# Optimization experiments

Hardware: AMD Instinct MI355X
Metric: run time of the kernel (lower is better)

Reference implementation:

```python
import jax, jax.numpy as jnp
import numpy as np

KS = 3
OFF = (KS - 1) // 2
KS2 = KS * KS


def _windows(xp, H, W):
    """xp: [..., H+KS-1, W+KS-1] -> [..., H, W, KS, KS] with flat index i = x*KS + y."""
    cols = [xp[..., x:x + H, y:y + W] for x in range(KS) for y in range(KS)]
    w = jnp.stack(cols, axis=-1)                      # [..., H, W, KS*KS]
    return w.reshape(w.shape[:-1] + (KS, KS))


def setup_inputs() -> dict:
    key = jax.random.key(0)
    k1, k2, k3, k4 = jax.random.split(key, 4)
    B, C, H = 8, 3, 512
    img = jax.random.uniform(k1, (B, C, H, H), dtype=jnp.float32) * 255.0
    noise = jax.random.uniform(k2, (B, C, H + 2 * OFF, H + 2 * OFF), dtype=jnp.float32)
    ids_sel = jax.random.randint(k3, (B,), 0, 2) > 0          # ~p selection mask
    ids_dilation_sel = jax.random.randint(k4, (B,), 0, 2) > 0  # ~p_mix mix mask
    return {"img": img, "noise": noise, "ids_sel": ids_sel,
            "ids_dilation_sel": ids_dilation_sel}


def reference(img, noise, ids_sel, ids_dilation_sel):
    B, C, H, W = img.shape
    imgf = img.astype(jnp.float32)
    # pad + additive uniform noise
    img_p = jnp.pad(imgf, ((0, 0), (0, 0), (OFF, OFF), (OFF, OFF))) + noise
    img_e = _windows(img_p, H, W)                     # [B,C,H,W,KS,KS]
    mean = img_e.mean(axis=(4, 5), keepdims=True)
    std = jnp.std(img_e, axis=(4, 5), ddof=1, keepdims=True)  # unbiased
    w = jnp.exp(-(img_e - mean) ** 2 / (2.0 * std ** 2))
    w3 = w.min(axis=1, keepdims=True)                 # [B,1,H,W,KS,KS]
    # first weighted average (sums channels in numerator, like the torch code)
    num = (img_e * w3).sum(axis=(1, 4, 5))            # [B,H,W]
    den = w3.sum(axis=(4, 5))[:, 0]                   # [B,H,W]
    img_r = num / den
    # sort-based pixel mixing: pick argmin (erosion) or argmax (dilation) index
    img_r_p = jnp.pad(img_r, ((0, 0), (OFF, OFF), (OFF, OFF)))
    img_r_e = _windows(img_r_p, H, W).reshape(B, H, W, KS2)
    ids_min = jnp.argmin(img_r_e, axis=3)
    ids_max = jnp.argmax(img_r_e, axis=3)
    ids_mix = jnp.where(ids_dilation_sel[:, None, None], ids_max, ids_min)
    w_flat = w3.reshape(B, H, W, KS2)
    w_mod = jnp.take_along_axis(w_flat, ids_mix[..., None], axis=3)[..., 0]  # [B,H,W]
    # second windowed weighted-average pass with the mixed weights
    w_mod_p = jnp.pad(w_mod, ((0, 0), (OFF, OFF), (OFF, OFF)))
    w_mod_e = _windows(w_mod_p, H, W)[:, None]        # [B,1,H,W,KS,KS]
    img_mod = (img_e * w_mod_e).sum(axis=(4, 5)) / w_mod_e.sum(axis=(4, 5))  # [B,C,H,W]
    out = jnp.where(ids_sel[:, None, None, None], img_mod, imgf)
    return out.astype(jnp.uint8)
```

## Files before the change

kernel.cpp:

```cpp
#include <hip/hip_runtime.h>
#include <hip/hip_fp16.h>

#define HH 512
#define WD 512
#define HP 514
#define BN 8
#define CN 3

#define TH 16
#define TW 32

#define SP_ROWS (TH + 6)
#define SP_COLS (TW + 6)
#define SR_ROWS (TH + 4)
#define SR_COLS (TW + 4)
#define SR_PITCH (SR_COLS + 1)
#define WM_ROWS (TH + 2)
#define WM_COLS (TW + 2)
#define WM_PITCH (WM_COLS + 1)
#define W9_STRIDE 10

__device__ __forceinline__ int load_flag(const int* __restrict__ p, int b) {
    bool all01 = true;
#pragma unroll
    for (int i = 0; i < BN; ++i) {
        int v = p[i];
        all01 = all01 && (v == 0 || v == 1);
    }
    if (all01) return p[b];
    const unsigned char* pb = (const unsigned char*)p;
    return pb[b] != 0;
}

__device__ __forceinline__ float fast_rcp(float x) {
    return __builtin_amdgcn_rcpf(x);
}

template <int P>
__device__ __forceinline__ void p2_pixel(const float4 (&col)[3][3], int r, int cc,
                                         bool hok, int w,
                                         float* __restrict__ sr,
                                         __half* __restrict__ w9) {
    float val = 0.f;
    if (hok && (unsigned)w < (unsigned)WD) {
        float sx = 0.f, sy = 0.f, sz = 0.f;
#pragma unroll
        for (int k = 0; k < 9; ++k) {
            const float4 tp = col[(k % 3 + P) % 3][k / 3];
            sx += tp.x; sy += tp.y; sz += tp.z;
        }
        float mx = sx * (1.f / 9.f), my = sy * (1.f / 9.f), mz = sz * (1.f / 9.f);
        float sdx = 0.f, sdy = 0.f, sdz = 0.f;
#pragma unroll
        for (int k = 0; k < 9; ++k) {
            const float4 tp = col[(k % 3 + P) % 3][k / 3];
            float dx = tp.x - mx, dy = tp.y - my, dz = tp.z - mz;
            sdx += dx * dx; sdy += dy * dy; sdz += dz * dz;
        }
        float ivx = 4.f * fast_rcp(sdx);
        float ivy = 4.f * fast_rcp(sdy);
        float ivz = 4.f * fast_rcp(sdz);
        float wk[9];
        float num = 0.f, den = 0.f;
#pragma unroll
        for (int k = 0; k < 9; ++k) {
            const float4 tp = col[(k % 3 + P) % 3][k / 3];
            float dx = tp.x - mx, dy = tp.y - my, dz = tp.z - mz;
            float txx = dx * dx * ivx, tyy = dy * dy * ivy, tzz = dz * dz * ivz;
            float m = fmaxf(txx, fmaxf(tyy, tzz));
            wk[k] = __expf(-m);
            num += (tp.x + tp.y + tp.z) * wk[k];
            den += wk[k];
        }
        val = num * fast_rcp(den);
        if (r >= 1 && r < SR_ROWS - 1 && cc >= 1 && cc < SR_COLS - 1) {
            int pix = (r - 1) * WM_COLS + (cc - 1);
            unsigned int* wp = (unsigned int*)&w9[pix * W9_STRIDE];
#pragma unroll
            for (int k = 0; k < 4; ++k) {
                __half2 h2 = __floats2half2_rn(wk[2 * k], wk[2 * k + 1]);
                wp[k] = *(unsigned int*)&h2;
            }
            w9[pix * W9_STRIDE + 8] = __float2half_rn(wk[8]);
        }
    }
    sr[r * SR_PITCH + cc] = val;
}

__global__ __launch_bounds__(256) void fused(const float* __restrict__ img,
                                             const float* __restrict__ noise,
                                             const int* __restrict__ ids_sel,
                                             const int* __restrict__ ids_dil,
                                             int* __restrict__ out) {
    int lin = blockIdx.x + 16 * blockIdx.y + 512 * blockIdx.z;
    int xcd = lin & 7;
    int m = lin >> 3;
    int b = m >> 6;
    int within = m & 63;
    int band = (xcd + b) & 7;
    int tl = band * 64 + within;
    int by = tl >> 4, bx = tl & 15;
    int h0 = by * TH, w0 = bx * TW;
    int t = threadIdx.x;

    if (!load_flag(ids_sel, b)) {
        int r = t >> 4, lx = (t & 15) << 1;
#pragma unroll
        for (int c = 0; c < CN; ++c) {
            const float* im = img + (size_t)(b * CN + c) * HH * WD;
            int* op = out + (size_t)(b * CN + c) * HH * WD;
            float2 v = *(const float2*)&im[(h0 + r) * WD + w0 + lx];
            int2 ov;
            ov.x = ((int)v.x) & 255;
            ov.y = ((int)v.y) & 255;
            __builtin_nontemporal_store(*(const long long*)&ov,
                                        (long long*)&op[(h0 + r) * WD + w0 + lx]);
        }
        return;
    }
    bool dil = load_flag(ids_dil, b) != 0;

    __shared__ float4 sp4[SP_ROWS * SP_COLS];
    __shared__ float sr[SR_ROWS * SR_PITCH];
    __shared__ float swm[WM_ROWS * WM_PITCH];
    __shared__ __align__(4) __half w9[WM_ROWS * WM_COLS * W9_STRIDE];

    {
        const float* nz = noise + (size_t)b * CN * HP * HP;
        const float* im = img + (size_t)b * CN * HH * WD;
        for (int idx = t; idx < SP_ROWS * SP_COLS; idx += 256) {
            int r = idx / SP_COLS, cc = idx - r * SP_COLS;
            int ip = h0 - 2 + r, jp = w0 - 2 + cc;
            ip = ip < 0 ? 0 : (ip > HP - 1 ? HP - 1 : ip);
            jp = jp < 0 ? 0 : (jp > HP - 1 ? HP - 1 : jp);
            bool in = (ip >= 1 && ip <= HH && jp >= 1 && jp <= WD);
            int no = ip * HP + jp;
            int io = (ip - 1) * WD + (jp - 1);
            float4 v;
            v.x = nz[no] + (in ? im[io] : 0.f);
            v.y = nz[HP * HP + no] + (in ? im[HH * WD + io] : 0.f);
            v.z = nz[2 * HP * HP + no] + (in ? im[2 * HH * WD + io] : 0.f);
            v.w = 0.f;
            sp4[idx] = v;
        }
    }
    __syncthreads();

    if (t < 240) {
        int r = t / 12;
        int s = t - r * 12;
        int cc0 = 3 * s;
        int h = h0 - 2 + r;
        bool hok = (h >= 0 && h < HH);
        float4 col[3][3];
#pragma unroll
        for (int j = 0; j < 3; ++j)
#pragma unroll
            for (int i = 0; i < 3; ++i)
                col[j][i] = sp4[(r + i) * SP_COLS + cc0 + j];
        p2_pixel<0>(col, r, cc0 + 0, hok, w0 - 2 + cc0 + 0, sr, w9);
#pragma unroll
        for (int i = 0; i < 3; ++i) col[0][i] = sp4[(r + i) * SP_COLS + cc0 + 3];
        p2_pixel<1>(col, r, cc0 + 1, hok, w0 - 2 + cc0 + 1, sr, w9);
#pragma unroll
        for (int i = 0; i < 3; ++i) col[1][i] = sp4[(r + i) * SP_COLS + cc0 + 4];
        p2_pixel<2>(col, r, cc0 + 2, hok, w0 - 2 + cc0 + 2, sr, w9);
    }
    __syncthreads();

    for (int idx = t; idx < WM_ROWS * WM_COLS; idx += 256) {
        int r = idx / WM_COLS, cc = idx - r * WM_COLS;
        int h = h0 - 1 + r, w = w0 - 1 + cc;
        float wmv = 0.f;
        if (h >= 0 && h < HH && w >= 0 && w < WD) {
            float rv[9];
#pragma unroll
            for (int k = 0; k < 9; ++k)
                rv[k] = sr[(r + k / 3) * SR_PITCH + cc + k % 3];
            int amin = 0, amax = 0;
            float vmin = rv[0], vmax = rv[0];
#pragma unroll
            for (int k = 1; k < 9; ++k) {
                if (rv[k] < vmin) { vmin = rv[k]; amin = k; }
                if (rv[k] > vmax) { vmax = rv[k]; amax = k; }
            }
            int ksel = dil ? amax : amin;
            wmv = __half2float(w9[idx * W9_STRIDE + ksel]);
        }
        swm[r * WM_PITCH + cc] = wmv;
    }
    __syncthreads();

    {
        int ly = t >> 4;
        int lx = (t & 15) << 1;
        float4 c4[3][3];
#pragma unroll
        for (int j = 0; j < 3; ++j)
#pragma unroll
            for (int i = 0; i < 3; ++i)
                c4[j][i] = sp4[(ly + 2 + i) * SP_COLS + lx + 2 + j];
        float ws[4][3];
#pragma unroll
        for (int j = 0; j < 4; ++j)
#pragma unroll
            for (int i = 0; i < 3; ++i)
                ws[j][i] = swm[(ly + i) * WM_PITCH + lx + j];
        int2 o0, o1, o2;
        {
            float den = 0.f, nx = 0.f, ny = 0.f, nz2 = 0.f;
#pragma unroll
            for (int k = 0; k < 9; ++k) {
                const float wkk = ws[k % 3][k / 3];
                const float4 tp = c4[k % 3][k / 3];
                den += wkk;
                nx += tp.x * wkk; ny += tp.y * wkk; nz2 += tp.z * wkk;
            }
            float rden = 1.f / den;
            o0.x = ((int)(nx * rden)) & 255;
            o1.x = ((int)(ny * rden)) & 255;
            o2.x = ((int)(nz2 * rden)) & 255;
        }
#pragma unroll
        for (int i = 0; i < 3; ++i) c4[0][i] = sp4[(ly + 2 + i) * SP_COLS + lx + 5];
        {
            float den = 0.f, nx = 0.f, ny = 0.f, nz2 = 0.f;
#pragma unroll
            for (int k = 0; k < 9; ++k) {
                const float wkk = ws[k % 3 + 1][k / 3];
                const float4 tp = c4[(k % 3 + 1) % 3][k / 3];
                den += wkk;
                nx += tp.x * wkk; ny += tp.y * wkk; nz2 += tp.z * wkk;
            }
            float rden = 1.f / den;
            o0.y = ((int)(nx * rden)) & 255;
            o1.y = ((int)(ny * rden)) & 255;
            o2.y = ((int)(nz2 * rden)) & 255;
        }
        size_t o = ((size_t)b * CN * HH + h0 + ly) * WD + w0 + lx;
        __builtin_nontemporal_store(*(const long long*)&o0, (long long*)&out[o]);
        __builtin_nontemporal_store(*(const long long*)&o1,
                                    (long long*)&out[o + (size_t)HH * WD]);
        __builtin_nontemporal_store(*(const long long*)&o2,
                                    (long long*)&out[o + 2 * (size_t)HH * WD]);
    }
}

extern "C" void kernel_launch(void* const* d_in, const int* in_sizes, int n_in,
                              void* d_out, int out_size, void* d_ws, size_t ws_size,
                              hipStream_t stream) {
    const float* img   = (const float*)d_in[0];
    const float* noise = (const float*)d_in[1];
    const int* ids_sel = (const int*)d_in[2];
    const int* ids_dil = (const int*)d_in[3];
    int* out = (int*)d_out;

    dim3 grid(WD / TW, HH / TH, BN);
    fused<<<grid, 256, 0, stream>>>(img, noise, ids_sel, ids_dil, out);
}
```

Before: 110.8 us.

## Shrink LDS footprint, batch nontemporal loads, and raise occupancy target

Drops the separate shared buffer for first-pass results and stores them in the unused w lane of the padded float4 tile. It also stores the mixed weights in half precision, which cuts LDS per block. The tile staging loop is restructured to issue all global loads (now nontemporal) for four iterations before any LDS stores, and launch bounds request 6 blocks per CU. The goal is higher occupancy and more memory-level parallelism. The risks are register pressure from the batched loads and the new occupancy hint, and extra LDS bank conflicts from the strided w-lane access.

New measurement: 111.3 us. No clear change (+0.5%).

```diff
diff --git a/kernel.cpp b/kernel.cpp
--- a/kernel.cpp
+++ b/kernel.cpp
@@ -14,12 +14,13 @@
 #define SP_COLS (TW + 6)
 #define SR_ROWS (TH + 4)
 #define SR_COLS (TW + 4)
-#define SR_PITCH (SR_COLS + 1)
 #define WM_ROWS (TH + 2)
 #define WM_COLS (TW + 2)
 #define WM_PITCH (WM_COLS + 1)
 #define W9_STRIDE 10
 
+typedef float f2v __attribute__((ext_vector_type(2)));
+
 __device__ __forceinline__ int load_flag(const int* __restrict__ p, int b) {
     bool all01 = true;
 #pragma unroll
@@ -36,10 +37,14 @@
     return __builtin_amdgcn_rcpf(x);
 }
 
+__device__ __forceinline__ float nt_load(const float* p) {
+    return __builtin_nontemporal_load(p);
+}
+
 template <int P>
 __device__ __forceinline__ void p2_pixel(const float4 (&col)[3][3], int r, int cc,
                                          bool hok, int w,
-                                         float* __restrict__ sr,
+                                         float* __restrict__ spw,
                                          __half* __restrict__ w9) {
     float val = 0.f;
     if (hok && (unsigned)w < (unsigned)WD) {
@@ -84,14 +89,14 @@
             w9[pix * W9_STRIDE + 8] = __float2half_rn(wk[8]);
         }
     }
-    sr[r * SR_PITCH + cc] = val;
-}
-
-__global__ __launch_bounds__(256) void fused(const float* __restrict__ img,
-                                             const float* __restrict__ noise,
-                                             const int* __restrict__ ids_sel,
-                                             const int* __restrict__ ids_dil,
-                                             int* __restrict__ out) {
+    spw[(r * SP_COLS + cc) * 4 + 3] = val;
+}
+
+__global__ __launch_bounds__(256, 6) void fused(const float* __restrict__ img,
+                                                const float* __restrict__ noise,
+                                                const int* __restrict__ ids_sel,
+                                                const int* __restrict__ ids_dil,
+                                                int* __restrict__ out) {
     int lin = blockIdx.x + 16 * blockIdx.y + 512 * blockIdx.z;
     int xcd = lin & 7;
     int m = lin >> 3;
@@ -109,7 +114,7 @@
         for (int c = 0; c < CN; ++c) {
             const float* im = img + (size_t)(b * CN + c) * HH * WD;
             int* op = out + (size_t)(b * CN + c) * HH * WD;
-            float2 v = *(const float2*)&im[(h0 + r) * WD + w0 + lx];
+            f2v v = __builtin_nontemporal_load((const f2v*)&im[(h0 + r) * WD + w0 + lx]);
             int2 ov;
             ov.x = ((int)v.x) & 255;
             ov.y = ((int)v.y) & 255;
@@ -121,27 +126,47 @@
     bool dil = load_flag(ids_dil, b) != 0;
 
     __shared__ float4 sp4[SP_ROWS * SP_COLS];
-    __shared__ float sr[SR_ROWS * SR_PITCH];
-    __shared__ float swm[WM_ROWS * WM_PITCH];
+    __shared__ __half swm[WM_ROWS * WM_PITCH];
     __shared__ __align__(4) __half w9[WM_ROWS * WM_COLS * W9_STRIDE];
+    float* spw = (float*)sp4;
 
     {
         const float* nz = noise + (size_t)b * CN * HP * HP;
         const float* im = img + (size_t)b * CN * HH * WD;
-        for (int idx = t; idx < SP_ROWS * SP_COLS; idx += 256) {
-            int r = idx / SP_COLS, cc = idx - r * SP_COLS;
-            int ip = h0 - 2 + r, jp = w0 - 2 + cc;
-            ip = ip < 0 ? 0 : (ip > HP - 1 ? HP - 1 : ip);
-            jp = jp < 0 ? 0 : (jp > HP - 1 ? HP - 1 : jp);
-            bool in = (ip >= 1 && ip <= HH && jp >= 1 && jp <= WD);
-            int no = ip * HP + jp;
-            int io = (ip - 1) * WD + (jp - 1);
-            float4 v;
-            v.x = nz[no] + (in ? im[io] : 0.f);
-            v.y = nz[HP * HP + no] + (in ? im[HH * WD + io] : 0.f);
-            v.z = nz[2 * HP * HP + no] + (in ? im[2 * HH * WD + io] : 0.f);
-            v.w = 0.f;
-            sp4[idx] = v;
+        float a0[4], a1[4], a2[4], b0[4], b1[4], b2[4];
+        int sidx[4];
+        bool act[4];
+#pragma unroll
+        for (int q = 0; q < 4; ++q) {
+            int idx = t + q * 256;
+            act[q] = idx < SP_ROWS * SP_COLS;
+            sidx[q] = idx;
+            if (act[q]) {
+                int r = idx / SP_COLS, cc = idx - r * SP_COLS;
+                int ip = h0 - 2 + r, jp = w0 - 2 + cc;
+                ip = ip < 0 ? 0 : (ip > HP - 1 ? HP - 1 : ip);
+                jp = jp < 0 ? 0 : (jp > HP - 1 ? HP - 1 : jp);
+                bool in = (ip >= 1 && ip <= HH && jp >= 1 && jp <= WD);
+                int no = ip * HP + jp;
+                int io = (ip - 1) * WD + (jp - 1);
+                a0[q] = nt_load(nz + no);
+                a1[q] = nt_load(nz + HP * HP + no);
+                a2[q] = nt_load(nz + 2 * HP * HP + no);
+                b0[q] = in ? nt_load(im + io) : 0.f;
+                b1[q] = in ? nt_load(im + HH * WD + io) : 0.f;
+                b2[q] = in ? nt_load(im + 2 * HH * WD + io) : 0.f;
+            }
+        }
+#pragma unroll
+        for (int q = 0; q < 4; ++q) {
+            if (act[q]) {
+                float4 v;
+                v.x = a0[q] + b0[q];
+                v.y = a1[q] + b1[q];
+                v.z = a2[q] + b2[q];
+                v.w = 0.f;
+                sp4[sidx[q]] = v;
+            }
         }
     }
     __syncthreads();
@@ -158,25 +183,25 @@
 #pragma unroll
             for (int i = 0; i < 3; ++i)
                 col[j][i] = sp4[(r + i) * SP_COLS + cc0 + j];
-        p2_pixel<0>(col, r, cc0 + 0, hok, w0 - 2 + cc0 + 0, sr, w9);
+        p2_pixel<0>(col, r, cc0 + 0, hok, w0 - 2 + cc0 + 0, spw, w9);
 #pragma unroll
         for (int i = 0; i < 3; ++i) col[0][i] = sp4[(r + i) * SP_COLS + cc0 + 3];
-        p2_pixel<1>(col, r, cc0 + 1, hok, w0 - 2 + cc0 + 1, sr, w9);
+        p2_pixel<1>(col, r, cc0 + 1, hok, w0 - 2 + cc0 + 1, spw, w9);
 #pragma unroll
         for (int i = 0; i < 3; ++i) col[1][i] = sp4[(r + i) * SP_COLS + cc0 + 4];
-        p2_pixel<2>(col, r, cc0 + 2, hok, w0 - 2 + cc0 + 2, sr, w9);
+        p2_pixel<2>(col, r, cc0 + 2, hok, w0 - 2 + cc0 + 2, spw, w9);
     }
     __syncthreads();
 
     for (int idx = t; idx < WM_ROWS * WM_COLS; idx += 256) {
         int r = idx / WM_COLS, cc = idx - r * WM_COLS;
         int h = h0 - 1 + r, w = w0 - 1 + cc;
-        float wmv = 0.f;
+        __half wmv = __ushort_as_half((unsigned short)0);
         if (h >= 0 && h < HH && w >= 0 && w < WD) {
             float rv[9];
 #pragma unroll
             for (int k = 0; k < 9; ++k)
-                rv[k] = sr[(r + k / 3) * SR_PITCH + cc + k % 3];
+                rv[k] = spw[((r + k / 3) * SP_COLS + cc + k % 3) * 4 + 3];
             int amin = 0, amax = 0;
             float vmin = rv[0], vmax = rv[0];
 #pragma unroll
@@ -185,7 +210,7 @@
                 if (rv[k] > vmax) { vmax = rv[k]; amax = k; }
             }
             int ksel = dil ? amax : amin;
-            wmv = __half2float(w9[idx * W9_STRIDE + ksel]);
+            wmv = w9[idx * W9_STRIDE + ksel];
         }
         swm[r * WM_PITCH + cc] = wmv;
     }
@@ -205,7 +230,7 @@
         for (int j = 0; j < 4; ++j)
 #pragma unroll
             for (int i = 0; i < 3; ++i)
-                ws[j][i] = swm[(ly + i) * WM_PITCH + lx + j];
+                ws[j][i] = __half2float(swm[(ly + i) * WM_PITCH + lx + j]);
         int2 o0, o1, o2;
         {
             float den = 0.f, nx = 0.f, ny = 0.f, nz2 = 0.f;
```

## Process two vertical tiles per block, prefetching second tile's loads into registers

Applied to the files above, without the earlier changes.

Each block now handles two vertically adjacent 16x32 tiles, halving the grid. The global loads for the second tile are issued into registers before phases 3 and 4 of the first tile run, so their latency overlaps with compute. The results are written to shared memory once the first tile is finished. Launch bounds now request 4 blocks per SM. This raises register pressure (24 prefetch floats per thread) and gives fewer blocks for load balancing, and the halo rows between the two tiles are still reloaded rather than reused.

Measured after the change: 110.6 us. About the same (-0.2%).

```diff
diff --git a/kernel.cpp b/kernel.cpp
--- a/kernel.cpp
+++ b/kernel.cpp
@@ -12,6 +12,7 @@
 
 #define SP_ROWS (TH + 6)
 #define SP_COLS (TW + 6)
+#define SP_N (SP_ROWS * SP_COLS)
 #define SR_ROWS (TH + 4)
 #define SR_COLS (TW + 4)
 #define SR_PITCH (SR_COLS + 1)
@@ -20,6 +21,8 @@
 #define WM_PITCH (WM_COLS + 1)
 #define W9_STRIDE 10
 
+typedef float f2v __attribute__((ext_vector_type(2)));
+
 __device__ __forceinline__ int load_flag(const int* __restrict__ p, int b) {
     bool all01 = true;
 #pragma unroll
@@ -34,6 +37,51 @@
 
 __device__ __forceinline__ float fast_rcp(float x) {
     return __builtin_amdgcn_rcpf(x);
+}
+
+struct P1R {
+    float a0[4], a1[4], a2[4];
+    float b0[4], b1[4], b2[4];
+};
+
+__device__ __forceinline__ void p1_issue(const float* __restrict__ nz,
+                                         const float* __restrict__ im,
+                                         int h0, int w0, int t, P1R& R) {
+#pragma unroll
+    for (int q = 0; q < 4; ++q) {
+        int idx = t + q * 256;
+        if (idx < SP_N) {
+            int r = idx / SP_COLS, cc = idx - r * SP_COLS;
+            int ip = h0 - 2 + r, jp = w0 - 2 + cc;
+            ip = ip < 0 ? 0 : (ip > HP - 1 ? HP - 1 : ip);
+            jp = jp < 0 ? 0 : (jp > HP - 1 ? HP - 1 : jp);
+            bool in = (ip >= 1 && ip <= HH && jp >= 1 && jp <= WD);
+            int no = ip * HP + jp;
+            int io = (ip - 1) * WD + (jp - 1);
+            R.a0[q] = nz[no];
+            R.a1[q] = nz[HP * HP + no];
+            R.a2[q] = nz[2 * HP * HP + no];
+            R.b0[q] = in ? im[io] : 0.f;
+            R.b1[q] = in ? im[HH * WD + io] : 0.f;
+            R.b2[q] = in ? im[2 * HH * WD + io] : 0.f;
+        }
+    }
+}
+
+__device__ __forceinline__ void p1_write(float4* __restrict__ sp4, int t,
+                                         const P1R& R) {
+#pragma unroll
+    for (int q = 0; q < 4; ++q) {
+        int idx = t + q * 256;
+        if (idx < SP_N) {
+            float4 v;
+            v.x = R.a0[q] + R.b0[q];
+            v.y = R.a1[q] + R.b1[q];
+            v.z = R.a2[q] + R.b2[q];
+            v.w = 0.f;
+            sp4[idx] = v;
+        }
+    }
 }
 
 template <int P>
@@ -87,65 +135,10 @@
     sr[r * SR_PITCH + cc] = val;
 }
 
-__global__ __launch_bounds__(256) void fused(const float* __restrict__ img,
-                                             const float* __restrict__ noise,
-                                             const int* __restrict__ ids_sel,
-                                             const int* __restrict__ ids_dil,
-                                             int* __restrict__ out) {
-    int lin = blockIdx.x + 16 * blockIdx.y + 512 * blockIdx.z;
-    int xcd = lin & 7;
-    int m = lin >> 3;
-    int b = m >> 6;
-    int within = m & 63;
-    int band = (xcd + b) & 7;
-    int tl = band * 64 + within;
-    int by = tl >> 4, bx = tl & 15;
-    int h0 = by * TH, w0 = bx * TW;
-    int t = threadIdx.x;
-
-    if (!load_flag(ids_sel, b)) {
-        int r = t >> 4, lx = (t & 15) << 1;
-#pragma unroll
-        for (int c = 0; c < CN; ++c) {
-            const float* im = img + (size_t)(b * CN + c) * HH * WD;
-            int* op = out + (size_t)(b * CN + c) * HH * WD;
-            float2 v = *(const float2*)&im[(h0 + r) * WD + w0 + lx];
-            int2 ov;
-            ov.x = ((int)v.x) & 255;
-            ov.y = ((int)v.y) & 255;
-            __builtin_nontemporal_store(*(const long long*)&ov,
-                                        (long long*)&op[(h0 + r) * WD + w0 + lx]);
-        }
-        return;
-    }
-    bool dil = load_flag(ids_dil, b) != 0;
-
-    __shared__ float4 sp4[SP_ROWS * SP_COLS];
-    __shared__ float sr[SR_ROWS * SR_PITCH];
-    __shared__ float swm[WM_ROWS * WM_PITCH];
-    __shared__ __align__(4) __half w9[WM_ROWS * WM_COLS * W9_STRIDE];
-
-    {
-        const float* nz = noise + (size_t)b * CN * HP * HP;
-        const float* im = img + (size_t)b * CN * HH * WD;
-        for (int idx = t; idx < SP_ROWS * SP_COLS; idx += 256) {
-            int r = idx / SP_COLS, cc = idx - r * SP_COLS;
-            int ip = h0 - 2 + r, jp = w0 - 2 + cc;
-            ip = ip < 0 ? 0 : (ip > HP - 1 ? HP - 1 : ip);
-            jp = jp < 0 ? 0 : (jp > HP - 1 ? HP - 1 : jp);
-            bool in = (ip >= 1 && ip <= HH && jp >= 1 && jp <= WD);
-            int no = ip * HP + jp;
-            int io = (ip - 1) * WD + (jp - 1);
-            float4 v;
-            v.x = nz[no] + (in ? im[io] : 0.f);
-            v.y = nz[HP * HP + no] + (in ? im[HH * WD + io] : 0.f);
-            v.z = nz[2 * HP * HP + no] + (in ? im[2 * HH * WD + io] : 0.f);
-            v.w = 0.f;
-            sp4[idx] = v;
-        }
-    }
-    __syncthreads();
-
+__device__ __forceinline__ void p2_phase(const float4* __restrict__ sp4,
+                                         float* __restrict__ sr,
+                                         __half* __restrict__ w9,
+                                         int h0, int w0, int t) {
     if (t < 240) {
         int r = t / 12;
         int s = t - r * 12;
@@ -166,8 +159,12 @@
         for (int i = 0; i < 3; ++i) col[1][i] = sp4[(r + i) * SP_COLS + cc0 + 4];
         p2_pixel<2>(col, r, cc0 + 2, hok, w0 - 2 + cc0 + 2, sr, w9);
     }
-    __syncthreads();
-
+}
+
+__device__ __forceinline__ void p3_phase(const float* __restrict__ sr,
+                                         const __half* __restrict__ w9,
+                                         float* __restrict__ swm,
+                                         int h0, int w0, int t, bool dil) {
     for (int idx = t; idx < WM_ROWS * WM_COLS; idx += 256) {
         int r = idx / WM_COLS, cc = idx - r * WM_COLS;
         int h = h0 - 1 + r, w = w0 - 1 + cc;
@@ -189,61 +186,132 @@
         }
         swm[r * WM_PITCH + cc] = wmv;
     }
-    __syncthreads();
-
+}
+
+__device__ __forceinline__ void p4_phase(const float4* __restrict__ sp4,
+                                         const float* __restrict__ swm,
+                                         int* __restrict__ out,
+                                         int b, int h0, int w0, int t) {
+    int ly = t >> 4;
+    int lx = (t & 15) << 1;
+    float4 c4[3][3];
+#pragma unroll
+    for (int j = 0; j < 3; ++j)
+#pragma unroll
+        for (int i = 0; i < 3; ++i)
+            c4[j][i] = sp4[(ly + 2 + i) * SP_COLS + lx + 2 + j];
+    float ws[4][3];
+#pragma unroll
+    for (int j = 0; j < 4; ++j)
+#pragma unroll
+        for (int i = 0; i < 3; ++i)
+            ws[j][i] = swm[(ly + i) * WM_PITCH + lx + j];
+    int2 o0, o1, o2;
     {
-        int ly = t >> 4;
-        int lx = (t & 15) << 1;
-        float4 c4[3][3];
-#pragma unroll
-        for (int j = 0; j < 3; ++j)
-#pragma unroll
-            for (int i = 0; i < 3; ++i)
-                c4[j][i] = sp4[(ly + 2 + i) * SP_COLS + lx + 2 + j];
-        float ws[4][3];
-#pragma unroll
-        for (int j = 0; j < 4; ++j)
-#pragma unroll
-            for (int i = 0; i < 3; ++i)
-                ws[j][i] = swm[(ly + i) * WM_PITCH + lx + j];
-        int2 o0, o1, o2;
-        {
-            float den = 0.f, nx = 0.f, ny = 0.f, nz2 = 0.f;
-#pragma unroll
-            for (int k = 0; k < 9; ++k) {
-                const float wkk = ws[k % 3][k / 3];
-                const float4 tp = c4[k % 3][k / 3];
-                den += wkk;
-                nx += tp.x * wkk; ny += tp.y * wkk; nz2 += tp.z * wkk;
+        float den = 0.f, nx = 0.f, ny = 0.f, nz2 = 0.f;
+#pragma unroll
+        for (int k = 0; k < 9; ++k) {
+            const float wkk = ws[k % 3][k / 3];
+            const float4 tp = c4[k % 3][k / 3];
+            den += wkk;
+            nx += tp.x * wkk; ny += tp.y * wkk; nz2 += tp.z * wkk;
+        }
+        float rden = 1.f / den;
+        o0.x = ((int)(nx * rden)) & 255;
+        o1.x = ((int)(ny * rden)) & 255;
+        o2.x = ((int)(nz2 * rden)) & 255;
+    }
+#pragma unroll
+    for (int i = 0; i < 3; ++i) c4[0][i] = sp4[(ly + 2 + i) * SP_COLS + lx + 5];
+    {
+        float den = 0.f, nx = 0.f, ny = 0.f, nz2 = 0.f;
+#pragma unroll
+        for (int k = 0; k < 9; ++k) {
+            const float wkk = ws[k % 3 + 1][k / 3];
+            const float4 tp = c4[(k % 3 + 1) % 3][k / 3];
+            den += wkk;
+            nx += tp.x * wkk; ny += tp.y * wkk; nz2 += tp.z * wkk;
+        }
+        float rden = 1.f / den;
+        o0.y = ((int)(nx * rden)) & 255;
+        o1.y = ((int)(ny * rden)) & 255;
+        o2.y = ((int)(nz2 * rden)) & 255;
+    }
+    size_t o = ((size_t)b * CN * HH + h0 + ly) * WD + w0 + lx;
+    __builtin_nontemporal_store(*(const long long*)&o0, (long long*)&out[o]);
+    __builtin_nontemporal_store(*(const long long*)&o1,
+                                (long long*)&out[o + (size_t)HH * WD]);
+    __builtin_nontemporal_store(*(const long long*)&o2,
+                                (long long*)&out[o + 2 * (size_t)HH * WD]);
+}
+
+__global__ __launch_bounds__(256, 4) void fused(const float* __restrict__ img,
+                                                const float* __restrict__ noise,
+                                                const int* __restrict__ ids_sel,
+                                                const int* __restrict__ ids_dil,
+                                                int* __restrict__ out) {
+    int lin = blockIdx.x + 16 * blockIdx.y + 256 * blockIdx.z;
+    int xcd = lin & 7;
+    int m = lin >> 3;
+    int b = m >> 5;
+    int within = m & 31;
+    int band = (xcd + b) & 7;
+    int tl = band * 32 + within;
+    int byp = tl >> 4, bx = tl & 15;
+    int h0A = (2 * byp) * TH, w0 = bx * TW;
+    int h0B = h0A + TH;
+    int t = threadIdx.x;
+
+    if (!load_flag(ids_sel, b)) {
+        int r = t >> 4, lx = (t & 15) << 1;
+#pragma unroll
+        for (int tt = 0; tt < 2; ++tt) {
+            int h0 = tt ? h0B : h0A;
+#pragma unroll
+            for (int c = 0; c < CN; ++c) {
+                const float* im = img + (size_t)(b * CN + c) * HH * WD;
+                int* op = out + (size_t)(b * CN + c) * HH * WD;
+                f2v v = *(const f2v*)&im[(h0 + r) * WD + w0 + lx];
+                int2 ov;
+                ov.x = ((int)v.x) & 255;
+                ov.y = ((int)v.y) & 255;
+                __builtin_nontemporal_store(*(const long long*)&ov,
+                                            (long long*)&op[(h0 + r) * WD + w0 + lx]);
             }
-            float rden = 1.f / den;
-            o0.x = ((int)(nx * rden)) & 255;
-            o1.x = ((int)(ny * rden)) & 255;
-            o2.x = ((int)(nz2 * rden)) & 255;
-        }
-#pragma unroll
-        for (int i = 0; i < 3; ++i) c4[0][i] = sp4[(ly + 2 + i) * SP_COLS + lx + 5];
-        {
-            float den = 0.f, nx = 0.f, ny = 0.f, nz2 = 0.f;
-#pragma unroll
-            for (int k = 0; k < 9; ++k) {
-                const float wkk = ws[k % 3 + 1][k / 3];
-                const float4 tp = c4[(k % 3 + 1) % 3][k / 3];
-                den += wkk;
-                nx += tp.x * wkk; ny += tp.y * wkk; nz2 += tp.z * wkk;
-            }
-            float rden = 1.f / den;
-            o0.y = ((int)(nx * rden)) & 255;
-            o1.y = ((int)(ny * rden)) & 255;
-            o2.y = ((int)(nz2 * rden)) & 255;
-        }
-        size_t o = ((size_t)b * CN * HH + h0 + ly) * WD + w0 + lx;
-        __builtin_nontemporal_store(*(const long long*)&o0, (long long*)&out[o]);
-        __builtin_nontemporal_store(*(const long long*)&o1,
-                                    (long long*)&out[o + (size_t)HH * WD]);
-        __builtin_nontemporal_store(*(const long long*)&o2,
-                                    (long long*)&out[o + 2 * (size_t)HH * WD]);
-    }
+        }
+        return;
+    }
+    bool dil = load_flag(ids_dil, b) != 0;
+
+    __shared__ float4 sp4[SP_N];
+    __shared__ float sr[SR_ROWS * SR_PITCH];
+    __shared__ float swm[WM_ROWS * WM_PITCH];
+    __shared__ __align__(4) __half w9[WM_ROWS * WM_COLS * W9_STRIDE];
+
+    const float* nz = noise + (size_t)b * CN * HP * HP;
+    const float* im = img + (size_t)b * CN * HH * WD;
+
+    {
+        P1R RA;
+        p1_issue(nz, im, h0A, w0, t, RA);
+        p1_write(sp4, t, RA);
+    }
+    __syncthreads();
+    p2_phase(sp4, sr, w9, h0A, w0, t);
+    __syncthreads();
+    P1R RB;
+    p1_issue(nz, im, h0B, w0, t, RB);
+    p3_phase(sr, w9, swm, h0A, w0, t, dil);
+    __syncthreads();
+    p4_phase(sp4, swm, out, b, h0A, w0, t);
+    __syncthreads();
+    p1_write(sp4, t, RB);
+    __syncthreads();
+    p2_phase(sp4, sr, w9, h0B, w0, t);
+    __syncthreads();
+    p3_phase(sr, w9, swm, h0B, w0, t, dil);
+    __syncthreads();
+    p4_phase(sp4, swm, out, b, h0B, w0, t);
 }
 
 extern "C" void kernel_launch(void* const* d_in, const int* in_sizes, int n_in,
@@ -255,6 +323,6 @@
     const int* ids_dil = (const int*)d_in[3];
     int* out = (int*)d_out;
 
-    dim3 grid(WD / TW, HH / TH, BN);
+    dim3 grid(WD / TW, HH / (2 * TH), BN);
     fused<<<grid, 256, 0, stream>>>(img, noise, ids_sel, ids_dil, out);
 }
```
